# Kernel tuning notes

Measured on AMD Instinct MI355X. Metric: run time of the kernel, lower is better.

The kernel has to match this reference:

```python
import jax, jax.numpy as jnp
import numpy as np

B, L, DX, H = 2, 2048, 1024, 16
DQ = DK = DV = DR = 64


def setup_inputs() -> dict:
    key0 = jax.random.key(0)
    ks = jax.random.split(key0, 14)
    def lin(kw, kb, din, dout):
        s = 1.0 / np.sqrt(din)
        w = jax.random.uniform(kw, (din, dout), jnp.float32, -s, s)
        b = jax.random.uniform(kb, (dout,), jnp.float32, -s, s)
        return w, b
    value = jax.random.normal(ks[0], (B, L, DX), jnp.float32)
    key_t = jax.random.normal(ks[1], (B, L, DX), jnp.float32)
    query = jax.random.normal(ks[2], (B, L, DX), jnp.float32)
    mask = jnp.tril(jnp.ones((L, L), jnp.int32))[None, None]  # [1,1,L,L] causal
    Wq_w, Wq_b = lin(ks[3], ks[4], DX, DQ * H)
    Wk_w, Wk_b = lin(ks[5], ks[6], DX, DK * H)
    Wv_w, Wv_b = lin(ks[7], ks[8], DX, DV * H)
    Wr_w, Wr_b = lin(ks[9], ks[10], DX, DR * H)
    wo_w, wo_b = lin(ks[11], ks[12], DV * H, DX)
    return dict(value=value, key=key_t, query=query, mask=mask,
                Wq_w=Wq_w, Wq_b=Wq_b, Wk_w=Wk_w, Wk_b=Wk_b,
                Wv_w=Wv_w, Wv_b=Wv_b, Wr_w=Wr_w, Wr_b=Wr_b,
                wo_w=wo_w, wo_b=wo_b)


def reference(value, key, query, mask, Wq_w, Wq_b, Wk_w, Wk_b, Wv_w, Wv_b,
              Wr_w, Wr_b, wo_w, wo_b):
    N, Lq, _ = query.shape
    q = (query @ Wq_w + Wq_b).reshape(N, Lq, H, DQ)   # nqhd
    k = (key @ Wk_w + Wk_b).reshape(N, -1, H, DK)     # nkhd
    v = (value @ Wv_w + Wv_b).reshape(N, -1, H, DV)   # nlhd
    r = (query @ Wr_w + Wr_b).reshape(N, Lq, H, DR)   # computed but unused (as in source)
    del r
    scores = jnp.einsum('nqhd,nkhd->nhqk', q, k)      # [N,H,L,L] materialized
    scores = jnp.where(mask == 0, jnp.float32(-1e20), scores)
    scale = jnp.float32(np.sqrt(DX))  # source divides by embedding_size**0.5
    attn = jax.nn.softmax(scores / scale, axis=3)
    out = jnp.einsum('nhql,nlhd->nqhd', attn, v).reshape(N, Lq, H * DV)
    return out @ wo_w + wo_b
```

## Files before the change

### kernel.cpp

```cpp
#include <hip/hip_runtime.h>
#include <hip/hip_bf16.h>
#include <type_traits>

typedef __hip_bfloat16 bf16;
typedef __attribute__((ext_vector_type(4))) float f32x4;
typedef __attribute__((ext_vector_type(8))) short s16x8;

#define DEVINL __device__ __forceinline__

#if defined(__has_builtin) && __has_builtin(__builtin_amdgcn_exp2f)
#define FEXP2(x) __builtin_amdgcn_exp2f(x)
#else
#define FEXP2(x) __exp2f(x)
#endif

DEVINL s16x8 load16B(const void* p) {
  s16x8 v;
  __builtin_memcpy(&v, __builtin_assume_aligned(p, 16), 16);
  return v;
}
DEVINL void store16B(void* p, s16x8 v) {
  __builtin_memcpy(__builtin_assume_aligned(p, 16), &v, 16);
}
DEVINL s16x8 cvt8(const float* p) {
  f32x4 a, b;
  __builtin_memcpy(&a, __builtin_assume_aligned(p, 16), 16);
  __builtin_memcpy(&b, __builtin_assume_aligned(p + 4, 16), 16);
  union { s16x8 v; bf16 h[8]; } u;
#pragma unroll
  for (int i = 0; i < 4; i++) {
    u.h[i] = __float2bfloat16(a[i]);
    u.h[4 + i] = __float2bfloat16(b[i]);
  }
  return u.v;
}
DEVINL void gload_lds16(const bf16* g, bf16* l) {
  __builtin_amdgcn_global_load_lds(
      (__attribute__((address_space(1))) void*)(void*)const_cast<bf16*>(g),
      (__attribute__((address_space(3))) void*)l, 16, 0, 0);
}

static constexpr int SEQ = 2048;
#define QSCALE 0.04508422002778011f

__global__ __launch_bounds__(256) void k_transpose(
    const float* __restrict__ Wq, const float* __restrict__ Wk,
    const float* __restrict__ Wv, const float* __restrict__ Wo,
    bf16* __restrict__ dst) {
  __shared__ float t[64][65];
  const float* src = blockIdx.z == 0 ? Wq : blockIdx.z == 1 ? Wk
                   : blockIdx.z == 2 ? Wv : Wo;
  bf16* out = dst + (size_t)blockIdx.z * 1024 * 1024;
  const int r0 = blockIdx.y * 64, c0 = blockIdx.x * 64;
#pragma unroll
  for (int i = 0; i < 16; i++) {
    int e = i * 256 + threadIdx.x;
    int r = e >> 6, c = e & 63;
    t[r][c] = src[(size_t)(r0 + r) * 1024 + c0 + c];
  }
  __syncthreads();
#pragma unroll
  for (int i = 0; i < 16; i++) {
    int e = i * 256 + threadIdx.x;
    int r = e >> 6, c = e & 63;
    out[(size_t)(c0 + r) * 1024 + r0 + c] = __float2bfloat16(t[c][r]);
  }
}

__global__ __launch_bounds__(256) void k_cvt3(
    const float* __restrict__ q, const float* __restrict__ k,
    const float* __restrict__ v, bf16* __restrict__ dstbase) {
  const float* src = blockIdx.z == 0 ? q : blockIdx.z == 1 ? k : v;
  bf16* dst = dstbase + (size_t)blockIdx.z * 4194304;
  size_t i = ((size_t)blockIdx.x * 256 + threadIdx.x) * 8;
  store16B(dst + i, cvt8(src + i));
}

template <typename XT, int MODE>
DEVINL void gemm_body(const XT* __restrict__ X, const bf16* __restrict__ WT,
                      const float* __restrict__ bias, void* __restrict__ dstv,
                      const float scale, const int m0, const int n0,
                      bf16* As, bf16* Bs) {
  const int tid = threadIdx.x;
  const int w = tid >> 6, lane = tid & 63, lg = lane >> 4, li = lane & 15;
  const int wm = w >> 1, wn = w & 1;

  f32x4 acc[4][4] = {};

  for (int kt = 0; kt < 32; ++kt) {
    const int k0 = kt * 32;
#pragma unroll
    for (int j = 0; j < 2; j++) {
      const int cb = (j * 4 + w) * 64;
      const int c = cb + lane;
      const int r = c >> 2, kk = (c & 3) * 8;
      gload_lds16(WT + (size_t)(n0 + r) * 1024 + k0 + kk, Bs + cb * 8);
      if constexpr (std::is_same_v<XT, bf16>)
        gload_lds16(X + (size_t)(m0 + r) * 1024 + k0 + kk, As + cb * 8);
    }
    if constexpr (std::is_same_v<XT, float>) {
#pragma unroll
      for (int j = 0; j < 2; j++) {
        const int c = j * 256 + tid;
        const int r = c >> 2, kk = (c & 3) * 8;
        s16x8 a = cvt8(X + (size_t)(m0 + r) * 1024 + k0 + kk);
        store16B((char*)As + c * 16, a);
      }
    }
    __syncthreads();
    s16x8 af[4], bfv[4];
#pragma unroll
    for (int i = 0; i < 4; i++)
      af[i] = load16B((char*)As + (wm * 64 + i * 16 + li) * 64 + lg * 16);
#pragma unroll
    for (int j = 0; j < 4; j++)
      bfv[j] = load16B((char*)Bs + (wn * 64 + j * 16 + li) * 64 + lg * 16);
#pragma unroll
    for (int i = 0; i < 4; i++)
#pragma unroll
      for (int j = 0; j < 4; j++) {
        if constexpr (MODE == 1)
          acc[i][j] = __builtin_amdgcn_mfma_f32_16x16x32_bf16(
              af[i], bfv[j], acc[i][j], 0, 0, 0);
        else
          acc[i][j] = __builtin_amdgcn_mfma_f32_16x16x32_bf16(
              bfv[j], af[i], acc[i][j], 0, 0, 0);
      }
    __syncthreads();
  }

  if constexpr (MODE == 1) {
    bf16* dst = (bf16*)dstv;
#pragma unroll
    for (int j = 0; j < 4; j++) {
      const int n = n0 + wn * 64 + j * 16 + li;
      const float bv = bias[n];
#pragma unroll
      for (int i = 0; i < 4; i++) {
        const int mrow = m0 + wm * 64 + i * 16 + lg * 4;
        f32x4 a = acc[i][j];
        size_t base =
            (((size_t)(mrow >> 11) * 16 + (n >> 6)) * 64 + (n & 63)) * SEQ +
            (mrow & 2047);
        bf16 tmp[4];
#pragma unroll
        for (int r = 0; r < 4; r++) tmp[r] = __float2bfloat16(a[r] + bv);
        __builtin_memcpy(__builtin_assume_aligned(dst + base, 8), tmp, 8);
      }
    }
  } else {
    f32x4 bias4[4];
#pragma unroll
    for (int j = 0; j < 4; j++)
      __builtin_memcpy(&bias4[j], bias + n0 + wn * 64 + j * 16 + lg * 4, 16);
#pragma unroll
    for (int i = 0; i < 4; i++) {
      const int m = m0 + wm * 64 + i * 16 + li;
      if constexpr (MODE == 2) {
        float* dst = (float*)dstv;
#pragma unroll
        for (int j = 0; j < 4; j++) {
          const int nb = n0 + wn * 64 + j * 16 + lg * 4;
          f32x4 v = acc[i][j] + bias4[j];
          __builtin_memcpy(__builtin_assume_aligned(
                               dst + (size_t)m * 1024 + nb, 16), &v, 16);
        }
      } else {
        bf16* dst = (bf16*)dstv;
        const int l = m & 2047, bb = m >> 11;
#pragma unroll
        for (int j = 0; j < 4; j++) {
          const int nb = n0 + wn * 64 + j * 16 + lg * 4;
          bf16 tmp[4];
#pragma unroll
          for (int r = 0; r < 4; r++)
            tmp[r] = __float2bfloat16((acc[i][j][r] + bias4[j][r]) * scale);
          size_t idx = (((size_t)bb * 16 + (nb >> 6)) * SEQ + l) * 64 +
                       (nb & 63);
          __builtin_memcpy(__builtin_assume_aligned(dst + idx, 8), tmp, 8);
        }
      }
    }
  }
}

__global__ __launch_bounds__(256) void k_gemm_qkv_bf16(
    const bf16* __restrict__ xbase, const bf16* __restrict__ WTbase,
    const float* __restrict__ qb, const float* __restrict__ kb,
    const float* __restrict__ vb, bf16* __restrict__ qo,
    bf16* __restrict__ ko, bf16* __restrict__ vto) {
  __shared__ alignas(16) bf16 As[128 * 32];
  __shared__ alignas(16) bf16 Bs[128 * 32];
  const int z = blockIdx.z;
  const bf16* X = xbase + (size_t)z * 4194304;
  const bf16* WT = WTbase + (size_t)z * 1048576;
  const float* bias = z == 0 ? qb : z == 1 ? kb : vb;
  if (z == 2)
    gemm_body<bf16, 1>(X, WT, bias, (void*)vto, 1.0f, blockIdx.x * 128,
                       blockIdx.y * 128, As, Bs);
  else
    gemm_body<bf16, 0>(X, WT, bias, z == 0 ? (void*)qo : (void*)ko,
                       z == 0 ? QSCALE : 1.0f, blockIdx.x * 128,
                       blockIdx.y * 128, As, Bs);
}

__global__ __launch_bounds__(256) void k_gemm_qkv_f32(
    const float* __restrict__ qx, const float* __restrict__ kx,
    const float* __restrict__ vx, const bf16* __restrict__ WTbase,
    const float* __restrict__ qb, const float* __restrict__ kb,
    const float* __restrict__ vb, bf16* __restrict__ qo,
    bf16* __restrict__ ko, bf16* __restrict__ vto) {
  __shared__ alignas(16) bf16 As[128 * 32];
  __shared__ alignas(16) bf16 Bs[128 * 32];
  const int z = blockIdx.z;
  const float* X = z == 0 ? qx : z == 1 ? kx : vx;
  const bf16* WT = WTbase + (size_t)z * 1048576;
  const float* bias = z == 0 ? qb : z == 1 ? kb : vb;
  if (z == 2)
    gemm_body<float, 1>(X, WT, bias, (void*)vto, 1.0f, blockIdx.x * 128,
                        blockIdx.y * 128, As, Bs);
  else
    gemm_body<float, 0>(X, WT, bias, z == 0 ? (void*)qo : (void*)ko,
                        z == 0 ? QSCALE : 1.0f, blockIdx.x * 128,
                        blockIdx.y * 128, As, Bs);
}

__global__ __launch_bounds__(256) void k_gemm_out(
    const bf16* __restrict__ X, const bf16* __restrict__ WT,
    const float* __restrict__ bias, float* __restrict__ out) {
  __shared__ alignas(16) bf16 As[128 * 32];
  __shared__ alignas(16) bf16 Bs[128 * 32];
  gemm_body<bf16, 2>(X, WT, bias, (void*)out, 1.0f, blockIdx.x * 128,
                     blockIdx.y * 128, As, Bs);
}

__global__ __launch_bounds__(256) void k_attn(
    const bf16* __restrict__ qb, const bf16* __restrict__ kb,
    const bf16* __restrict__ vtb, bf16* __restrict__ attn) {
  __shared__ alignas(16) bf16 Ks[2][64 * 64];
  __shared__ alignas(16) bf16 Vts[2][64 * 64];
  __shared__ alignas(16) bf16 Ps[4][16 * 64];
  const int tid = threadIdx.x;
  const int w = tid >> 6, lane = tid & 63, lg = lane >> 4, li = lane & 15;
  const int bh = blockIdx.x;
  const int y = blockIdx.y;
  const int qblk = (y < 8) ? 31 - y : (y < 16) ? y + 8
                 : (y < 24) ? 31 - y : y - 24;
  const int qrow = qblk * 64 + w * 16;
  const bf16* qh = qb + (size_t)bh * SEQ * 64;
  const bf16* kh = kb + (size_t)bh * SEQ * 64;
  const bf16* vth = vtb + (size_t)bh * 64 * SEQ;

  s16x8 aq[2];
#pragma unroll
  for (int c = 0; c < 2; c++)
    aq[c] = load16B(qh + (size_t)(qrow + li) * 64 + c * 32 + lg * 8);

  f32x4 o[4] = {};
  float m_run = -1e38f;
  float l_run = 0.f;

  const int c0s = tid, c1s = 256 + tid;
  const int by0 = (c0s * 16) ^ (((c0s >> 3) & 7) << 4);
  const int by1 = (c1s * 16) ^ (((c1s >> 3) & 7) << 4);
  const int d0 = c0s >> 3, kk0 = (c0s & 7) * 8;
  const int d1 = c1s >> 3, kk1 = (c1s & 7) * 8;
  const int psw = (li & 7) << 3;

  s16x8 rk[2], rv[2];
  rk[0] = load16B(kh + (size_t)c0s * 8);
  rk[1] = load16B(kh + (size_t)c1s * 8);
  rv[0] = load16B(vth + (size_t)d0 * SEQ + kk0);
  rv[1] = load16B(vth + (size_t)d1 * SEQ + kk1);
  store16B((char*)Ks[0] + by0, rk[0]);
  store16B((char*)Ks[0] + by1, rk[1]);
  store16B((char*)Vts[0] + by0, rv[0]);
  store16B((char*)Vts[0] + by1, rv[1]);
  if (qblk >= 1) {
    rk[0] = load16B(kh + (size_t)64 * 64 + c0s * 8);
    rk[1] = load16B(kh + (size_t)64 * 64 + c1s * 8);
    rv[0] = load16B(vth + (size_t)d0 * SEQ + 64 + kk0);
    rv[1] = load16B(vth + (size_t)d1 * SEQ + 64 + kk1);
  }
  __syncthreads();

  for (int kbk = 0; kbk <= qblk; ++kbk) {
    const int cur = kbk & 1;
    if (kbk < qblk) {
      store16B((char*)Ks[cur ^ 1] + by0, rk[0]);
      store16B((char*)Ks[cur ^ 1] + by1, rk[1]);
      store16B((char*)Vts[cur ^ 1] + by0, rv[0]);
      store16B((char*)Vts[cur ^ 1] + by1, rv[1]);
      if (kbk + 2 <= qblk) {
        const int kn = (kbk + 2) * 64;
        rk[0] = load16B(kh + (size_t)kn * 64 + c0s * 8);
        rk[1] = load16B(kh + (size_t)kn * 64 + c1s * 8);
        rv[0] = load16B(vth + (size_t)d0 * SEQ + kn + kk0);
        rv[1] = load16B(vth + (size_t)d1 * SEQ + kn + kk1);
      }
    }

    f32x4 s[4];
    __builtin_amdgcn_s_setprio(1);
#pragma unroll
    for (int t = 0; t < 4; t++) {
      f32x4 z = {};
#pragma unroll
      for (int c = 0; c < 2; c++) {
        int row = t * 16 + li;
        s16x8 ak = load16B((char*)Ks[cur] +
                           ((row * 128 + c * 64 + lg * 16) ^ ((row & 7) << 4)));
        z = __builtin_amdgcn_mfma_f32_16x16x32_bf16(ak, aq[c], z, 0, 0, 0);
      }
      s[t] = z;
    }
    __builtin_amdgcn_s_setprio(0);

    if (kbk == qblk) {
      const int kb0 = kbk * 64 + lg * 4;
      const int qg = qrow + li;
#pragma unroll
      for (int t = 0; t < 4; t++)
#pragma unroll
        for (int r = 0; r < 4; r++)
          if (kb0 + t * 16 + r > qg) s[t][r] = -1e30f;
    }

    f32x4 mm = s[0];
#pragma unroll
    for (int t = 1; t < 4; t++)
#pragma unroll
      for (int r = 0; r < 4; r++) mm[r] = fmaxf(mm[r], s[t][r]);
    float mr = fmaxf(fmaxf(mm[0], mm[1]), fmaxf(mm[2], mm[3]));
    mr = fmaxf(mr, __shfl_xor(mr, 16));
    mr = fmaxf(mr, __shfl_xor(mr, 32));

    const bool grow = !__all(mr <= m_run + 8.0f);
    const float mn = grow ? fmaxf(m_run, mr) : m_run;

    float p[4][4];
    float s0 = 0.f, s1 = 0.f, s2 = 0.f, s3 = 0.f;
#pragma unroll
    for (int r = 0; r < 4; r++) {
      float p0 = FEXP2(s[0][r] - mn), p1 = FEXP2(s[1][r] - mn);
      float p2 = FEXP2(s[2][r] - mn), p3 = FEXP2(s[3][r] - mn);
      p[0][r] = p0; p[1][r] = p1; p[2][r] = p2; p[3][r] = p3;
      s0 += p0; s1 += p1; s2 += p2; s3 += p3;
    }
    float sum = (s0 + s1) + (s2 + s3);
    sum += __shfl_xor(sum, 16);
    sum += __shfl_xor(sum, 32);

    if (grow) {
      const float cr = FEXP2(m_run - mn);
      l_run = l_run * cr + sum;
      m_run = mn;
      const int sb = (lane & 48);
      float crr[4];
#pragma unroll
      for (int r = 0; r < 4; r++) crr[r] = __shfl(cr, sb + (sb >> 2) + r);
#pragma unroll
      for (int t = 0; t < 4; t++)
#pragma unroll
        for (int r = 0; r < 4; r++) o[t][r] *= crr[r];
    } else {
      l_run += sum;
    }

#pragma unroll
    for (int t = 0; t < 4; t++) {
      bf16 tmp[4];
#pragma unroll
      for (int r = 0; r < 4; r++) tmp[r] = __float2bfloat16(p[t][r]);
      __builtin_memcpy(
          __builtin_assume_aligned(
              &Ps[w][li * 64 + ((t * 16 + lg * 4) ^ psw)], 8),
          tmp, 8);
    }

    s16x8 ap[2];
#pragma unroll
    for (int c = 0; c < 2; c++)
      ap[c] = load16B(&Ps[w][li * 64 + ((c * 32 + lg * 8) ^ psw)]);

    __builtin_amdgcn_s_setprio(1);
#pragma unroll
    for (int t = 0; t < 4; t++) {
#pragma unroll
      for (int c = 0; c < 2; c++) {
        int row = t * 16 + li;
        s16x8 bv = load16B((char*)Vts[cur] +
                           ((row * 128 + c * 64 + lg * 16) ^ ((row & 7) << 4)));
        o[t] = __builtin_amdgcn_mfma_f32_16x16x32_bf16(ap[c], bv, o[t], 0, 0, 0);
      }
    }
    __builtin_amdgcn_s_setprio(0);
    __syncthreads();
  }

  const int b = bh >> 4, h = bh & 15;
  const float inv = 1.0f / l_run;
  const int sb = (lane & 48);
  float invr[4];
#pragma unroll
  for (int r = 0; r < 4; r++) invr[r] = __shfl(inv, sb + (sb >> 2) + r);
#pragma unroll
  for (int r = 0; r < 4; r++)
#pragma unroll
    for (int t = 0; t < 4; t++) {
      size_t idx = (size_t)(b * SEQ + qrow + lg * 4 + r) * 1024 + h * 64 +
                   t * 16 + li;
      attn[idx] = __float2bfloat16(o[t][r] * invr[r]);
    }
}

extern "C" void kernel_launch(void* const* d_in, const int* in_sizes, int n_in,
                              void* d_out, int out_size, void* d_ws,
                              size_t ws_size, hipStream_t stream) {
  (void)in_sizes; (void)n_in; (void)out_size;
  const float* value = (const float*)d_in[0];
  const float* key   = (const float*)d_in[1];
  const float* query = (const float*)d_in[2];
  const float* Wq_w = (const float*)d_in[4];
  const float* Wq_b = (const float*)d_in[5];
  const float* Wk_w = (const float*)d_in[6];
  const float* Wk_b = (const float*)d_in[7];
  const float* Wv_w = (const float*)d_in[8];
  const float* Wv_b = (const float*)d_in[9];
  const float* wo_w = (const float*)d_in[12];
  const float* wo_b = (const float*)d_in[13];

  bf16* ws = (bf16*)d_ws;
  const size_t MM = 1048576;
  bf16* WT = ws;

  k_transpose<<<dim3(16, 16, 4), 256, 0, stream>>>(Wq_w, Wk_w, Wv_w, wo_w, WT);

  if (ws_size >= 28ull * MM * 2) {
    bf16* xbuf = ws + 4 * MM;
    bf16* qbuf = ws + 16 * MM;
    bf16* kbuf = ws + 20 * MM;
    bf16* vtbf = ws + 24 * MM;
    bf16* abuf = ws + 4 * MM;
    k_cvt3<<<dim3(2048, 1, 3), 256, 0, stream>>>(query, key, value, xbuf);
    k_gemm_qkv_bf16<<<dim3(32, 8, 3), 256, 0, stream>>>(
        xbuf, WT, Wq_b, Wk_b, Wv_b, qbuf, kbuf, vtbf);
    k_attn<<<dim3(32, 32), 256, 0, stream>>>(qbuf, kbuf, vtbf, abuf);
    k_gemm_out<<<dim3(32, 8), 256, 0, stream>>>(abuf, WT + 3 * MM, wo_b,
                                                (float*)d_out);
  } else {
    bf16* qbuf = ws + 4 * MM;
    bf16* kbuf = ws + 8 * MM;
    bf16* vtbf = ws + 12 * MM;
    bf16* abuf = ws + 16 * MM;
    k_gemm_qkv_f32<<<dim3(32, 8, 3), 256, 0, stream>>>(
        query, key, value, WT, Wq_b, Wk_b, Wv_b, qbuf, kbuf, vtbf);
    k_attn<<<dim3(32, 32), 256, 0, stream>>>(qbuf, kbuf, vtbf, abuf);
    k_gemm_out<<<dim3(32, 8), 256, 0, stream>>>(abuf, WT + 3 * MM, wo_b,
                                                (float*)d_out);
  }
}
```

Before: 127.5 us.

## Pair complementary causal query blocks per attention workgroup and transpose output GEMM epilogue

```diff
diff --git a/kernel.cpp b/kernel.cpp
--- a/kernel.cpp
+++ b/kernel.cpp
@@ -119,12 +119,12 @@
     for (int i = 0; i < 4; i++)
 #pragma unroll
       for (int j = 0; j < 4; j++) {
-        if constexpr (MODE == 1)
+        if constexpr (MODE == 0)
+          acc[i][j] = __builtin_amdgcn_mfma_f32_16x16x32_bf16(
+              bfv[j], af[i], acc[i][j], 0, 0, 0);
+        else
           acc[i][j] = __builtin_amdgcn_mfma_f32_16x16x32_bf16(
               af[i], bfv[j], acc[i][j], 0, 0, 0);
-        else
-          acc[i][j] = __builtin_amdgcn_mfma_f32_16x16x32_bf16(
-              bfv[j], af[i], acc[i][j], 0, 0, 0);
       }
     __syncthreads();
   }
@@ -148,37 +148,40 @@
         __builtin_memcpy(__builtin_assume_aligned(dst + base, 8), tmp, 8);
       }
     }
+  } else if constexpr (MODE == 2) {
+    float* dst = (float*)dstv;
+#pragma unroll
+    for (int j = 0; j < 4; j++) {
+      const int n = n0 + wn * 64 + j * 16 + li;
+      const float bv = bias[n];
+#pragma unroll
+      for (int i = 0; i < 4; i++) {
+        const int mrow = m0 + wm * 64 + i * 16 + lg * 4;
+        f32x4 a = acc[i][j];
+#pragma unroll
+        for (int r = 0; r < 4; r++)
+          dst[(size_t)(mrow + r) * 1024 + n] = a[r] + bv;
+      }
+    }
   } else {
     f32x4 bias4[4];
 #pragma unroll
     for (int j = 0; j < 4; j++)
       __builtin_memcpy(&bias4[j], bias + n0 + wn * 64 + j * 16 + lg * 4, 16);
+    bf16* dst = (bf16*)dstv;
 #pragma unroll
     for (int i = 0; i < 4; i++) {
       const int m = m0 + wm * 64 + i * 16 + li;
-      if constexpr (MODE == 2) {
-        float* dst = (float*)dstv;
-#pragma unroll
-        for (int j = 0; j < 4; j++) {
-          const int nb = n0 + wn * 64 + j * 16 + lg * 4;
-          f32x4 v = acc[i][j] + bias4[j];
-          __builtin_memcpy(__builtin_assume_aligned(
-                               dst + (size_t)m * 1024 + nb, 16), &v, 16);
-        }
-      } else {
-        bf16* dst = (bf16*)dstv;
-        const int l = m & 2047, bb = m >> 11;
-#pragma unroll
-        for (int j = 0; j < 4; j++) {
-          const int nb = n0 + wn * 64 + j * 16 + lg * 4;
-          bf16 tmp[4];
-#pragma unroll
-          for (int r = 0; r < 4; r++)
-            tmp[r] = __float2bfloat16((acc[i][j][r] + bias4[j][r]) * scale);
-          size_t idx = (((size_t)bb * 16 + (nb >> 6)) * SEQ + l) * 64 +
-                       (nb & 63);
-          __builtin_memcpy(__builtin_assume_aligned(dst + idx, 8), tmp, 8);
-        }
+      const int l = m & 2047, bb = m >> 11;
+#pragma unroll
+      for (int j = 0; j < 4; j++) {
+        const int nb = n0 + wn * 64 + j * 16 + lg * 4;
+        bf16 tmp[4];
+#pragma unroll
+        for (int r = 0; r < 4; r++)
+          tmp[r] = __float2bfloat16((acc[i][j][r] + bias4[j][r]) * scale);
+        size_t idx = (((size_t)bb * 16 + (nb >> 6)) * SEQ + l) * 64 + (nb & 63);
+        __builtin_memcpy(__builtin_assume_aligned(dst + idx, 8), tmp, 8);
       }
     }
   }
@@ -244,21 +247,9 @@
   const int w = tid >> 6, lane = tid & 63, lg = lane >> 4, li = lane & 15;
   const int bh = blockIdx.x;
   const int y = blockIdx.y;
-  const int qblk = (y < 8) ? 31 - y : (y < 16) ? y + 8
-                 : (y < 24) ? 31 - y : y - 24;
-  const int qrow = qblk * 64 + w * 16;
   const bf16* qh = qb + (size_t)bh * SEQ * 64;
   const bf16* kh = kb + (size_t)bh * SEQ * 64;
   const bf16* vth = vtb + (size_t)bh * 64 * SEQ;
-
-  s16x8 aq[2];
-#pragma unroll
-  for (int c = 0; c < 2; c++)
-    aq[c] = load16B(qh + (size_t)(qrow + li) * 64 + c * 32 + lg * 8);
-
-  f32x4 o[4] = {};
-  float m_run = -1e38f;
-  float l_run = 0.f;
 
   const int c0s = tid, c1s = 256 + tid;
   const int by0 = (c0s * 16) ^ (((c0s >> 3) & 7) << 4);
@@ -266,152 +257,169 @@
   const int d0 = c0s >> 3, kk0 = (c0s & 7) * 8;
   const int d1 = c1s >> 3, kk1 = (c1s & 7) * 8;
   const int psw = (li & 7) << 3;
-
-  s16x8 rk[2], rv[2];
-  rk[0] = load16B(kh + (size_t)c0s * 8);
-  rk[1] = load16B(kh + (size_t)c1s * 8);
-  rv[0] = load16B(vth + (size_t)d0 * SEQ + kk0);
-  rv[1] = load16B(vth + (size_t)d1 * SEQ + kk1);
-  store16B((char*)Ks[0] + by0, rk[0]);
-  store16B((char*)Ks[0] + by1, rk[1]);
-  store16B((char*)Vts[0] + by0, rv[0]);
-  store16B((char*)Vts[0] + by1, rv[1]);
-  if (qblk >= 1) {
-    rk[0] = load16B(kh + (size_t)64 * 64 + c0s * 8);
-    rk[1] = load16B(kh + (size_t)64 * 64 + c1s * 8);
-    rv[0] = load16B(vth + (size_t)d0 * SEQ + 64 + kk0);
-    rv[1] = load16B(vth + (size_t)d1 * SEQ + 64 + kk1);
-  }
-  __syncthreads();
-
-  for (int kbk = 0; kbk <= qblk; ++kbk) {
-    const int cur = kbk & 1;
-    if (kbk < qblk) {
-      store16B((char*)Ks[cur ^ 1] + by0, rk[0]);
-      store16B((char*)Ks[cur ^ 1] + by1, rk[1]);
-      store16B((char*)Vts[cur ^ 1] + by0, rv[0]);
-      store16B((char*)Vts[cur ^ 1] + by1, rv[1]);
-      if (kbk + 2 <= qblk) {
-        const int kn = (kbk + 2) * 64;
-        rk[0] = load16B(kh + (size_t)kn * 64 + c0s * 8);
-        rk[1] = load16B(kh + (size_t)kn * 64 + c1s * 8);
-        rv[0] = load16B(vth + (size_t)d0 * SEQ + kn + kk0);
-        rv[1] = load16B(vth + (size_t)d1 * SEQ + kn + kk1);
-      }
-    }
-
-    f32x4 s[4];
-    __builtin_amdgcn_s_setprio(1);
-#pragma unroll
-    for (int t = 0; t < 4; t++) {
-      f32x4 z = {};
-#pragma unroll
-      for (int c = 0; c < 2; c++) {
-        int row = t * 16 + li;
-        s16x8 ak = load16B((char*)Ks[cur] +
-                           ((row * 128 + c * 64 + lg * 16) ^ ((row & 7) << 4)));
-        z = __builtin_amdgcn_mfma_f32_16x16x32_bf16(ak, aq[c], z, 0, 0, 0);
-      }
-      s[t] = z;
-    }
-    __builtin_amdgcn_s_setprio(0);
-
-    if (kbk == qblk) {
-      const int kb0 = kbk * 64 + lg * 4;
-      const int qg = qrow + li;
-#pragma unroll
-      for (int t = 0; t < 4; t++)
-#pragma unroll
-        for (int r = 0; r < 4; r++)
-          if (kb0 + t * 16 + r > qg) s[t][r] = -1e30f;
-    }
-
-    f32x4 mm = s[0];
-#pragma unroll
-    for (int t = 1; t < 4; t++)
-#pragma unroll
-      for (int r = 0; r < 4; r++) mm[r] = fmaxf(mm[r], s[t][r]);
-    float mr = fmaxf(fmaxf(mm[0], mm[1]), fmaxf(mm[2], mm[3]));
-    mr = fmaxf(mr, __shfl_xor(mr, 16));
-    mr = fmaxf(mr, __shfl_xor(mr, 32));
-
-    const bool grow = !__all(mr <= m_run + 8.0f);
-    const float mn = grow ? fmaxf(m_run, mr) : m_run;
-
-    float p[4][4];
-    float s0 = 0.f, s1 = 0.f, s2 = 0.f, s3 = 0.f;
-#pragma unroll
-    for (int r = 0; r < 4; r++) {
-      float p0 = FEXP2(s[0][r] - mn), p1 = FEXP2(s[1][r] - mn);
-      float p2 = FEXP2(s[2][r] - mn), p3 = FEXP2(s[3][r] - mn);
-      p[0][r] = p0; p[1][r] = p1; p[2][r] = p2; p[3][r] = p3;
-      s0 += p0; s1 += p1; s2 += p2; s3 += p3;
-    }
-    float sum = (s0 + s1) + (s2 + s3);
-    sum += __shfl_xor(sum, 16);
-    sum += __shfl_xor(sum, 32);
-
-    if (grow) {
-      const float cr = FEXP2(m_run - mn);
-      l_run = l_run * cr + sum;
-      m_run = mn;
-      const int sb = (lane & 48);
-      float crr[4];
-#pragma unroll
-      for (int r = 0; r < 4; r++) crr[r] = __shfl(cr, sb + (sb >> 2) + r);
-#pragma unroll
-      for (int t = 0; t < 4; t++)
-#pragma unroll
-        for (int r = 0; r < 4; r++) o[t][r] *= crr[r];
-    } else {
-      l_run += sum;
-    }
-
-#pragma unroll
-    for (int t = 0; t < 4; t++) {
-      bf16 tmp[4];
-#pragma unroll
-      for (int r = 0; r < 4; r++) tmp[r] = __float2bfloat16(p[t][r]);
-      __builtin_memcpy(
-          __builtin_assume_aligned(
-              &Ps[w][li * 64 + ((t * 16 + lg * 4) ^ psw)], 8),
-          tmp, 8);
-    }
-
-    s16x8 ap[2];
+  const int b = bh >> 4, h = bh & 15;
+  const int sb = (lane & 48);
+
+#pragma unroll
+  for (int half = 0; half < 2; half++) {
+    const int qblk = half == 0 ? 31 - y : y;
+    const int qrow = qblk * 64 + w * 16;
+
+    s16x8 aq[2];
 #pragma unroll
     for (int c = 0; c < 2; c++)
-      ap[c] = load16B(&Ps[w][li * 64 + ((c * 32 + lg * 8) ^ psw)]);
-
-    __builtin_amdgcn_s_setprio(1);
-#pragma unroll
-    for (int t = 0; t < 4; t++) {
-#pragma unroll
-      for (int c = 0; c < 2; c++) {
-        int row = t * 16 + li;
-        s16x8 bv = load16B((char*)Vts[cur] +
-                           ((row * 128 + c * 64 + lg * 16) ^ ((row & 7) << 4)));
-        o[t] = __builtin_amdgcn_mfma_f32_16x16x32_bf16(ap[c], bv, o[t], 0, 0, 0);
-      }
-    }
-    __builtin_amdgcn_s_setprio(0);
+      aq[c] = load16B(qh + (size_t)(qrow + li) * 64 + c * 32 + lg * 8);
+
+    f32x4 o[4] = {};
+    float m_run = -1e38f;
+    float l_run = 0.f;
+
+    s16x8 rk[2], rv[2];
+    rk[0] = load16B(kh + (size_t)c0s * 8);
+    rk[1] = load16B(kh + (size_t)c1s * 8);
+    rv[0] = load16B(vth + (size_t)d0 * SEQ + kk0);
+    rv[1] = load16B(vth + (size_t)d1 * SEQ + kk1);
+    store16B((char*)Ks[0] + by0, rk[0]);
+    store16B((char*)Ks[0] + by1, rk[1]);
+    store16B((char*)Vts[0] + by0, rv[0]);
+    store16B((char*)Vts[0] + by1, rv[1]);
+    if (qblk >= 1) {
+      rk[0] = load16B(kh + (size_t)64 * 64 + c0s * 8);
+      rk[1] = load16B(kh + (size_t)64 * 64 + c1s * 8);
+      rv[0] = load16B(vth + (size_t)d0 * SEQ + 64 + kk0);
+      rv[1] = load16B(vth + (size_t)d1 * SEQ + 64 + kk1);
+    }
     __syncthreads();
-  }
-
-  const int b = bh >> 4, h = bh & 15;
-  const float inv = 1.0f / l_run;
-  const int sb = (lane & 48);
-  float invr[4];
-#pragma unroll
-  for (int r = 0; r < 4; r++) invr[r] = __shfl(inv, sb + (sb >> 2) + r);
-#pragma unroll
-  for (int r = 0; r < 4; r++)
-#pragma unroll
-    for (int t = 0; t < 4; t++) {
-      size_t idx = (size_t)(b * SEQ + qrow + lg * 4 + r) * 1024 + h * 64 +
-                   t * 16 + li;
-      attn[idx] = __float2bfloat16(o[t][r] * invr[r]);
-    }
+
+    for (int kbk = 0; kbk <= qblk; ++kbk) {
+      const int cur = kbk & 1;
+      if (kbk < qblk) {
+        store16B((char*)Ks[cur ^ 1] + by0, rk[0]);
+        store16B((char*)Ks[cur ^ 1] + by1, rk[1]);
+        store16B((char*)Vts[cur ^ 1] + by0, rv[0]);
+        store16B((char*)Vts[cur ^ 1] + by1, rv[1]);
+        if (kbk + 2 <= qblk) {
+          const int kn = (kbk + 2) * 64;
+          rk[0] = load16B(kh + (size_t)kn * 64 + c0s * 8);
+          rk[1] = load16B(kh + (size_t)kn * 64 + c1s * 8);
+          rv[0] = load16B(vth + (size_t)d0 * SEQ + kn + kk0);
+          rv[1] = load16B(vth + (size_t)d1 * SEQ + kn + kk1);
+        }
+      }
+
+      f32x4 s[4];
+      __builtin_amdgcn_s_setprio(1);
+#pragma unroll
+      for (int t = 0; t < 4; t++) {
+        f32x4 z = {};
+#pragma unroll
+        for (int c = 0; c < 2; c++) {
+          int row = t * 16 + li;
+          s16x8 ak =
+              load16B((char*)Ks[cur] +
+                      ((row * 128 + c * 64 + lg * 16) ^ ((row & 7) << 4)));
+          z = __builtin_amdgcn_mfma_f32_16x16x32_bf16(ak, aq[c], z, 0, 0, 0);
+        }
+        s[t] = z;
+      }
+      __builtin_amdgcn_s_setprio(0);
+
+      if (kbk == qblk) {
+        const int kb0 = kbk * 64 + lg * 4;
+        const int qg = qrow + li;
+#pragma unroll
+        for (int t = 0; t < 4; t++)
+#pragma unroll
+          for (int r = 0; r < 4; r++)
+            if (kb0 + t * 16 + r > qg) s[t][r] = -1e30f;
+      }
+
+      f32x4 mm = s[0];
+#pragma unroll
+      for (int t = 1; t < 4; t++)
+#pragma unroll
+        for (int r = 0; r < 4; r++) mm[r] = fmaxf(mm[r], s[t][r]);
+      float mr = fmaxf(fmaxf(mm[0], mm[1]), fmaxf(mm[2], mm[3]));
+      mr = fmaxf(mr, __shfl_xor(mr, 16));
+      mr = fmaxf(mr, __shfl_xor(mr, 32));
+
+      const bool grow = !__all(mr <= m_run + 8.0f);
+      const float mn = grow ? fmaxf(m_run, mr) : m_run;
+
+      float p[4][4];
+      float s0 = 0.f, s1 = 0.f, s2 = 0.f, s3 = 0.f;
+#pragma unroll
+      for (int r = 0; r < 4; r++) {
+        float p0 = FEXP2(s[0][r] - mn), p1 = FEXP2(s[1][r] - mn);
+        float p2 = FEXP2(s[2][r] - mn), p3 = FEXP2(s[3][r] - mn);
+        p[0][r] = p0; p[1][r] = p1; p[2][r] = p2; p[3][r] = p3;
+        s0 += p0; s1 += p1; s2 += p2; s3 += p3;
+      }
+      float sum = (s0 + s1) + (s2 + s3);
+      sum += __shfl_xor(sum, 16);
+      sum += __shfl_xor(sum, 32);
+
+      if (grow) {
+        const float cr = FEXP2(m_run - mn);
+        l_run = l_run * cr + sum;
+        m_run = mn;
+        float crr[4];
+#pragma unroll
+        for (int r = 0; r < 4; r++) crr[r] = __shfl(cr, sb + (sb >> 2) + r);
+#pragma unroll
+        for (int t = 0; t < 4; t++)
+#pragma unroll
+          for (int r = 0; r < 4; r++) o[t][r] *= crr[r];
+      } else {
+        l_run += sum;
+      }
+
+#pragma unroll
+      for (int t = 0; t < 4; t++) {
+        bf16 tmp[4];
+#pragma unroll
+        for (int r = 0; r < 4; r++) tmp[r] = __float2bfloat16(p[t][r]);
+        __builtin_memcpy(
+            __builtin_assume_aligned(
+                &Ps[w][li * 64 + ((t * 16 + lg * 4) ^ psw)], 8),
+            tmp, 8);
+      }
+
+      s16x8 ap[2];
+#pragma unroll
+      for (int c = 0; c < 2; c++)
+        ap[c] = load16B(&Ps[w][li * 64 + ((c * 32 + lg * 8) ^ psw)]);
+
+      __builtin_amdgcn_s_setprio(1);
+#pragma unroll
+      for (int t = 0; t < 4; t++) {
+#pragma unroll
+        for (int c = 0; c < 2; c++) {
+          int row = t * 16 + li;
+          s16x8 bv =
+              load16B((char*)Vts[cur] +
+                      ((row * 128 + c * 64 + lg * 16) ^ ((row & 7) << 4)));
+          o[t] =
+              __builtin_amdgcn_mfma_f32_16x16x32_bf16(ap[c], bv, o[t], 0, 0, 0);
+        }
+      }
+      __builtin_amdgcn_s_setprio(0);
+      __syncthreads();
+    }
+
+    const float inv = 1.0f / l_run;
+    float invr[4];
+#pragma unroll
+    for (int r = 0; r < 4; r++) invr[r] = __shfl(inv, sb + (sb >> 2) + r);
+#pragma unroll
+    for (int r = 0; r < 4; r++)
+#pragma unroll
+      for (int t = 0; t < 4; t++) {
+        size_t idx = (size_t)(b * SEQ + qrow + lg * 4 + r) * 1024 + h * 64 +
+                     t * 16 + li;
+        attn[idx] = __float2bfloat16(o[t][r] * invr[r]);
+      }
+  }
 }
 
 extern "C" void kernel_launch(void* const* d_in, const int* in_sizes, int n_in,
@@ -445,7 +453,7 @@
     k_cvt3<<<dim3(2048, 1, 3), 256, 0, stream>>>(query, key, value, xbuf);
     k_gemm_qkv_bf16<<<dim3(32, 8, 3), 256, 0, stream>>>(
         xbuf, WT, Wq_b, Wk_b, Wv_b, qbuf, kbuf, vtbf);
-    k_attn<<<dim3(32, 32), 256, 0, stream>>>(qbuf, kbuf, vtbf, abuf);
+    k_attn<<<dim3(32, 16), 256, 0, stream>>>(qbuf, kbuf, vtbf, abuf);
     k_gemm_out<<<dim3(32, 8), 256, 0, stream>>>(abuf, WT + 3 * MM, wo_b,
                                                 (float*)d_out);
   } else {
@@ -455,7 +463,7 @@
     bf16* abuf = ws + 16 * MM;
     k_gemm_qkv_f32<<<dim3(32, 8, 3), 256, 0, stream>>>(
         query, key, value, WT, Wq_b, Wk_b, Wv_b, qbuf, kbuf, vtbf);
-    k_attn<<<dim3(32, 32), 256, 0, stream>>>(qbuf, kbuf, vtbf, abuf);
+    k_attn<<<dim3(32, 16), 256, 0, stream>>>(qbuf, kbuf, vtbf, abuf);
     k_gemm_out<<<dim3(32, 8), 256, 0, stream>>>(abuf, WT + 3 * MM, wo_b,
                                                 (float*)d_out);
   }
```

Measured after the change: 126.7 us. About the same (-0.6%).
